# Kernel optimization log

Hardware: AMD Instinct MI355X
Metric: run time of the kernel (lower is better)

## Reference

```python
import jax, jax.numpy as jnp
import numpy as np

N = 100000       # n_entities + n_users
E = 1000000      # edges
D = 64           # entity_dim (phase/mod half-width)
R = 40           # n_relations
PI = 3.1415926235897933
GAMMA = 12.0
EMB_RANGE = (GAMMA + 2.0) / D   # (gamma + epsilon) / entity_dim
DIMS = [128, 64, 32, 16]        # conv_dim_list = [2*D] + [64,32,16]


def setup_inputs() -> dict:
    key = jax.random.key(0)
    ks = jax.random.split(key, 20)
    inp = {}
    inp["entity_embed"] = jax.random.uniform(ks[0], (N, 2 * D), minval=-EMB_RANGE, maxval=EMB_RANGE, dtype=jnp.float32)
    inp["rel_embed"] = jax.random.uniform(ks[1], (R, 3 * D), minval=-EMB_RANGE, maxval=EMB_RANGE, dtype=jnp.float32)
    inp["phase_w"] = jnp.array([[0.5 * EMB_RANGE]], dtype=jnp.float32)
    inp["mod_w"] = jnp.array([[1.0]], dtype=jnp.float32)
    names = [("W1_0", "b1_0", "W2_0", "b2_0"), ("W1_1", "b1_1", "W2_1", "b2_1"), ("W1_2", "b1_2", "W1_2b", "b2_2")]
    for i, (w1n, b1n, w2n, b2n) in enumerate(names):
        din, dout = DIMS[i], DIMS[i + 1]
        s = 1.0 / np.sqrt(din)
        inp[w1n] = jax.random.uniform(ks[2 + 4 * i], (dout, din), minval=-s, maxval=s, dtype=jnp.float32)
        inp[b1n] = jax.random.uniform(ks[3 + 4 * i], (dout,), minval=-s, maxval=s, dtype=jnp.float32)
        inp[w2n] = jax.random.uniform(ks[4 + 4 * i], (dout, din), minval=-s, maxval=s, dtype=jnp.float32)
        inp[b2n] = jax.random.uniform(ks[5 + 4 * i], (dout,), minval=-s, maxval=s, dtype=jnp.float32)
    inp["src"] = jax.random.randint(ks[14], (E,), 0, N, dtype=jnp.int32)
    inp["dst"] = jax.random.randint(ks[15], (E,), 0, N, dtype=jnp.int32)
    inp["etype"] = jax.random.randint(ks[16], (E,), 0, R, dtype=jnp.int32)
    return inp


def _edge_att(entity_embed, rel_embed, phase_w, mod_w, src, dst, etype):
    # HAKE att_score: h = dst node, t = src node (per original code)
    h = entity_embed[dst]            # [E, 2D]
    t = entity_embed[src]            # [E, 2D]
    r = rel_embed[etype]             # [E, 3D]
    scale = EMB_RANGE / PI
    ph, mh = h[:, :D], h[:, D:]
    pr, mr, br = r[:, :D], r[:, D:2 * D], r[:, 2 * D:]
    pt, mt = t[:, :D], t[:, D:]
    mr = jnp.abs(mr)
    br = jnp.minimum(br, 1.0)
    br = jnp.where(br < -mr, -mr, br)  # conditional write bias_relation[indicator] = -mod_relation
    mod_score = jnp.linalg.norm(mh * (mr + br) - mt * (1.0 - br), axis=1) * mod_w[0, 0]
    phase = (ph + pr - pt) / scale
    phase_score = jnp.sum(jnp.abs(jnp.sin(phase / 2.0)), axis=1) * phase_w[0, 0]
    att = phase_score + mod_score    # [E]
    # edge softmax over incoming edges of each dst node
    amax = jax.ops.segment_max(att, dst, num_segments=N)
    ex = jnp.exp(att - amax[dst])
    den = jax.ops.segment_sum(ex, dst, num_segments=N)
    return ex / den[dst]


def reference(entity_embed, rel_embed, phase_w, mod_w,
              W1_0, b1_0, W2_0, b2_0,
              W1_1, b1_1, W2_1, b2_1,
              W1_2, b1_2, W1_2b, b2_2,
              src, dst, etype):
    att = _edge_att(entity_embed, rel_embed, phase_w, mod_w, src, dst, etype)

    def layer(node, W1, b1, W2, b2):
        # u_mul_e('node','att','side') + sum('side','N_h')
        msg = node[src] * att[:, None]                    # [E, din]
        Nh = jax.ops.segment_sum(msg, dst, num_segments=N)
        # bi-interaction aggregator
        o = jax.nn.leaky_relu((node + Nh) @ W1.T + b1) + jax.nn.leaky_relu((node * Nh) @ W2.T + b2)
        nrm = jnp.linalg.norm(o, axis=1, keepdims=True)
        return o, o / jnp.maximum(nrm, 1e-12)             # (ego_embed, F.normalize)

    ego = entity_embed
    outs = [ego]
    for (W1, b1, W2, b2) in [(W1_0, b1_0, W2_0, b2_0), (W1_1, b1_1, W2_1, b2_1), (W1_2, b1_2, W1_2b, b2_2)]:
        ego, normed = layer(ego, W1, b1, W2, b2)
        outs.append(normed)
    return jnp.concatenate(outs, axis=1)                   # [N, 128+64+32+16]
```

## Files before the change

kernel.cpp:

```cpp
#include <hip/hip_runtime.h>
#include <math.h>


__global__ void hist_kernel(const int* __restrict__ dst, int* __restrict__ cnt,
                            int nedges) {
    int e = blockIdx.x * blockDim.x + threadIdx.x;
    if (e < nedges) atomicAdd(&cnt[dst[e]], 1);
}

__global__ __launch_bounds__(1024) void scan_block_kernel(
    const int* __restrict__ cnt, int* __restrict__ rowptr,
    int* __restrict__ bsum, int n) {
    __shared__ int swv[16];
    int tid = threadIdx.x, lane = tid & 63, wid = tid >> 6;
    int i = blockIdx.x * 1024 + tid;
    int v = (i < n) ? cnt[i] : 0;
    #pragma unroll
    for (int off = 1; off < 64; off <<= 1) {
        int t = __shfl_up(v, off, 64);
        if (lane >= off) v += t;
    }
    if (lane == 63) swv[wid] = v;
    __syncthreads();
    if (wid == 0) {
        int s = (lane < 16) ? swv[lane] : 0;
        #pragma unroll
        for (int off = 1; off < 16; off <<= 1) {
            int t = __shfl_up(s, off, 64);
            if (lane >= off) s += t;
        }
        if (lane < 16) swv[lane] = s;
    }
    __syncthreads();
    int offv = wid ? swv[wid - 1] : 0;
    if (i < n) rowptr[i + 1] = v + offv;
    if (tid == 1023) bsum[blockIdx.x] = v + offv;
}

__global__ __launch_bounds__(64) void scan_tops_kernel(
    const int* __restrict__ bsum, int* __restrict__ boff, int nb) {
    int l = threadIdx.x;
    int a = (2 * l < nb) ? bsum[2 * l] : 0;
    int b = (2 * l + 1 < nb) ? bsum[2 * l + 1] : 0;
    int s = a + b;
    #pragma unroll
    for (int off = 1; off < 64; off <<= 1) {
        int t = __shfl_up(s, off, 64);
        if (l >= off) s += t;
    }
    int excl = s - (a + b);
    if (2 * l < nb) boff[2 * l] = excl;
    if (2 * l + 1 < nb) boff[2 * l + 1] = excl + a;
}

__global__ __launch_bounds__(1024) void scan_add_kernel(
    int* __restrict__ rowptr, const int* __restrict__ boff, int n) {
    int i = blockIdx.x * 1024 + threadIdx.x;
    if (i < n) rowptr[i + 1] += boff[blockIdx.x];
    if (i == 0) rowptr[0] = 0;
}

__global__ void fill_kernel(const int* __restrict__ src, const int* __restrict__ dst,
                            const int* __restrict__ etype,
                            const int* __restrict__ rowptr, int* __restrict__ cursor,
                            int* __restrict__ se_s, int nedges) {
    int e = blockIdx.x * blockDim.x + threadIdx.x;
    if (e >= nedges) return;
    int d = dst[e];
    int slot = rowptr[d] + atomicAdd(&cursor[d], 1);
    se_s[slot] = src[e] | (etype[e] << 17);
}

__global__ __launch_bounds__(512) void att_gather_kernel(
    const float* __restrict__ embed, const float* __restrict__ rel,
    const float* __restrict__ pw, const float* __restrict__ mw,
    const int* __restrict__ se_s, const int* __restrict__ rowptr,
    float* __restrict__ att_s, float* __restrict__ ai,
    float* __restrict__ Nh, int nnodes, int nrel)
{
    __shared__ float sRel[40 * 196];
    int tid = threadIdx.x;

    for (int idx = tid; idx < nrel * 64; idx += 512) {
        int r = idx >> 6, d = idx & 63;
        float pr = rel[r * 192 + d];
        float mr = fabsf(rel[r * 192 + 64 + d]);
        float br = rel[r * 192 + 128 + d];
        br = fminf(br, 1.0f);
        br = fmaxf(br, -mr);
        sRel[r * 196 + d]       = mr + br;
        sRel[r * 196 + 64 + d]  = 1.0f - br;
        sRel[r * 196 + 128 + d] = pr;
    }
    __syncthreads();

    const float K = (float)(0.5 * 3.1415926235897933 / 0.21875);
    float mwv = mw[0], pwv = pw[0];

    int wave = tid >> 6, lane = tid & 63;
    int g = lane >> 4;
    int q = lane & 15;

    for (int v = blockIdx.x * 8 + wave; v < nnodes; v += gridDim.x * 8) {
        int beg = rowptr[v];
        int deg = rowptr[v + 1] - beg;

        const float* hrow = embed + (size_t)v * 128;
        float4 hp = *(const float4*)(hrow + 4 * q);
        float4 hm = *(const float4*)(hrow + 64 + 4 * q);

        float den = 0.0f;
        float4 accp = make_float4(0.f, 0.f, 0.f, 0.f);
        float4 accm = make_float4(0.f, 0.f, 0.f, 0.f);

        for (int kb = 0; kb < deg; kb += 64) {
            int kchunk = min(64, deg - kb);
            int sev = (lane < kchunk) ? se_s[beg + kb + lane] : 0;

            bool valid0 = g < kchunk;
            int se0 = __shfl(sev, valid0 ? g : 0, 64);
            int r0 = se0 >> 17;
            const float* trow0 = embed + (size_t)(se0 & 0x1FFFF) * 128;
            float4 tp0 = *(const float4*)(trow0 + 4 * q);
            float4 tm0 = *(const float4*)(trow0 + 64 + 4 * q);

            for (int k0 = 0; k0 < kchunk; k0 += 4) {
                float4 tp1 = tp0, tm1 = tm0;
                int r1 = r0;
                bool valid1 = false;
                if (k0 + 4 < kchunk) {
                    int kn = k0 + 4 + g;
                    valid1 = kn < kchunk;
                    int se1 = __shfl(sev, valid1 ? kn : 0, 64);
                    r1 = se1 >> 17;
                    const float* trow1 = embed + (size_t)(se1 & 0x1FFFF) * 128;
                    tp1 = *(const float4*)(trow1 + 4 * q);
                    tm1 = *(const float4*)(trow1 + 64 + 4 * q);
                }

                const float* rrow = sRel + r0 * 196;
                float4 A4 = *(const float4*)(rrow + 4 * q);
                float4 B4 = *(const float4*)(rrow + 64 + 4 * q);
                float4 P4 = *(const float4*)(rrow + 128 + 4 * q);

                float pp;
                pp  = fabsf(__sinf((hp.x + P4.x - tp0.x) * K));
                pp += fabsf(__sinf((hp.y + P4.y - tp0.y) * K));
                pp += fabsf(__sinf((hp.z + P4.z - tp0.z) * K));
                pp += fabsf(__sinf((hp.w + P4.w - tp0.w) * K));

                float d0 = hm.x * A4.x - tm0.x * B4.x;
                float d1 = hm.y * A4.y - tm0.y * B4.y;
                float d2 = hm.z * A4.z - tm0.z * B4.z;
                float d3 = hm.w * A4.w - tm0.w * B4.w;
                float qq = (d0 * d0 + d1 * d1) + (d2 * d2 + d3 * d3);

                #pragma unroll
                for (int off = 1; off < 16; off <<= 1) {
                    pp += __shfl_xor(pp, off, 64);
                    qq += __shfl_xor(qq, off, 64);
                }
                float s = sqrtf(qq) * mwv + pp * pwv;
                float w = valid0 ? __expf(s) : 0.0f;
                den += w;
                accp.x = fmaf(w, tp0.x, accp.x); accp.y = fmaf(w, tp0.y, accp.y);
                accp.z = fmaf(w, tp0.z, accp.z); accp.w = fmaf(w, tp0.w, accp.w);
                accm.x = fmaf(w, tm0.x, accm.x); accm.y = fmaf(w, tm0.y, accm.y);
                accm.z = fmaf(w, tm0.z, accm.z); accm.w = fmaf(w, tm0.w, accm.w);
                if (valid0 && q == 0) att_s[beg + kb + k0 + g] = w;

                tp0 = tp1; tm0 = tm1; r0 = r1; valid0 = valid1;
            }
        }

        #pragma unroll
        for (int off = 16; off < 64; off <<= 1) {
            accp.x += __shfl_xor(accp.x, off, 64);
            accp.y += __shfl_xor(accp.y, off, 64);
            accp.z += __shfl_xor(accp.z, off, 64);
            accp.w += __shfl_xor(accp.w, off, 64);
            accm.x += __shfl_xor(accm.x, off, 64);
            accm.y += __shfl_xor(accm.y, off, 64);
            accm.z += __shfl_xor(accm.z, off, 64);
            accm.w += __shfl_xor(accm.w, off, 64);
            den += __shfl_xor(den, off, 64);
        }
        float invd = (deg > 0) ? 1.0f / den : 0.0f;
        if (g == 0) {
            float* pn = Nh + (size_t)v * 128;
            *(float4*)(pn + 4 * q) = make_float4(accp.x * invd, accp.y * invd,
                                                 accp.z * invd, accp.w * invd);
            *(float4*)(pn + 64 + 4 * q) = make_float4(accm.x * invd, accm.y * invd,
                                                      accm.z * invd, accm.w * invd);
            if (q == 0) ai[v] = invd;
        }
    }
}

template<int DIN>
__global__ __launch_bounds__(256) void gather_kernel(
    const float* __restrict__ node, int nstride, const float* __restrict__ nrm,
    const float* __restrict__ att_s, const int* __restrict__ se_s,
    const int* __restrict__ rowptr, const float* __restrict__ ai,
    float* __restrict__ Nh, int nnodes)
{
    constexpr int LPE = DIN / 4;
    constexpr int EP  = 64 / LPE;
    constexpr int U   = 4;
    int v = blockIdx.x * 4 + (threadIdx.x >> 6);
    if (v >= nnodes) return;
    int lane = threadIdx.x & 63;
    int sub = lane / LPE;
    int c = lane % LPE;
    int beg = rowptr[v];
    int deg = rowptr[v + 1] - beg;

    float4 acc = make_float4(0.f, 0.f, 0.f, 0.f);
    for (int kb = 0; kb < deg; kb += 64) {
        int kc = kb + lane;
        bool inr = kc < deg;
        int sv = inr ? (se_s[beg + kc] & 0x1FFFF) : 0;
        float av = inr ? att_s[beg + kc] * nrm[sv] : 0.0f;
        int kmax = min(64, deg - kb);
        for (int k0 = 0; k0 < kmax; k0 += U * EP) {
            float a[U];
            const float4* p[U];
            #pragma unroll
            for (int u = 0; u < U; ++u) {
                int kk = k0 + u * EP + sub;
                bool val = kk < kmax;
                int kidx = val ? kk : 0;
                int ssrc = __shfl(sv, kidx, 64);
                float aa = __shfl(av, kidx, 64);
                a[u] = val ? aa : 0.0f;
                p[u] = (const float4*)(node + (size_t)ssrc * nstride + 4 * c);
            }
            float4 rv[U];
            #pragma unroll
            for (int u = 0; u < U; ++u) rv[u] = *p[u];
            #pragma unroll
            for (int u = 0; u < U; ++u) {
                acc.x += a[u] * rv[u].x;
                acc.y += a[u] * rv[u].y;
                acc.z += a[u] * rv[u].z;
                acc.w += a[u] * rv[u].w;
            }
        }
    }
    #pragma unroll
    for (int off = LPE; off < 64; off <<= 1) {
        acc.x += __shfl_xor(acc.x, off, 64);
        acc.y += __shfl_xor(acc.y, off, 64);
        acc.z += __shfl_xor(acc.z, off, 64);
        acc.w += __shfl_xor(acc.w, off, 64);
    }
    if (sub == 0) {
        float aiv = ai[v];
        float4 o = make_float4(acc.x * aiv, acc.y * aiv,
                               acc.z * aiv, acc.w * aiv);
        *(float4*)(Nh + (size_t)v * DIN + 4 * c) = o;
    }
}

template<int DIN, int DOUT, bool NRM, bool EGO>
__global__ __launch_bounds__(512) void gemm_kernel(
    const float* __restrict__ node, int nstride, const float* __restrict__ nrm_in,
    const float* __restrict__ Nh,
    const float* __restrict__ W1, const float* __restrict__ b1,
    const float* __restrict__ W2, const float* __restrict__ b2,
    float* __restrict__ out, int out_col, float* __restrict__ nrm_out, int nnodes)
{
    constexpr int IH  = (DIN < 64) ? DIN : 64;
    constexpr int NHV = DIN / IH;
    constexpr int XS  = IH + 1;
    constexpr int CPR = IH / 8;
    constexpr int DH  = DOUT / 8;
    __shared__ float sx1[64 * XS], sx2[64 * XS];
    __shared__ float sred[8][64];

    int tid = threadIdx.x;
    int tile0 = blockIdx.x * 64;
    int lane = tid & 63;
    int jh = __builtin_amdgcn_readfirstlane(tid >> 6);
    int j0 = jh * DH;
    int v = tile0 + lane;
    bool act = v < nnodes;

    float acc1[DH], acc2[DH];
    #pragma unroll
    for (int j = 0; j < DH; ++j) { acc1[j] = 0.f; acc2[j] = 0.f; }

    const float* px1 = sx1 + lane * XS;
    const float* px2 = sx2 + lane * XS;

    #pragma unroll
    for (int h = 0; h < NHV; ++h) {
        const int i0 = h * IH;
        if (h) __syncthreads();

        for (int idx = tid; idx < 64 * CPR; idx += 512) {
            int row = idx / CPR, c = idx % CPR;
            int vv = tile0 + row;
            float4 n0 = make_float4(0.f, 0.f, 0.f, 0.f), n1 = n0;
            float4 h0 = n0, h1 = n0;
            if (vv < nnodes) {
                const float* pn = node + (size_t)vv * nstride + i0 + 8 * c;
                const float* ph = Nh + (size_t)vv * DIN + i0 + 8 * c;
                n0 = *(const float4*)pn;
                n1 = *(const float4*)(pn + 4);
                h0 = *(const float4*)ph;
                h1 = *(const float4*)(ph + 4);
                if (EGO) {
                    float* po = out + (size_t)vv * 240 + i0 + 8 * c;
                    *(float4*)po = n0;
                    *(float4*)(po + 4) = n1;
                }
                if (NRM) {
                    float rn = nrm_in[vv];
                    n0.x *= rn; n0.y *= rn; n0.z *= rn; n0.w *= rn;
                    n1.x *= rn; n1.y *= rn; n1.z *= rn; n1.w *= rn;
                }
            }
            float* p1 = sx1 + row * XS + 8 * c;
            float* p2 = sx2 + row * XS + 8 * c;
            p1[0] = n0.x + h0.x; p1[1] = n0.y + h0.y;
            p1[2] = n0.z + h0.z; p1[3] = n0.w + h0.w;
            p1[4] = n1.x + h1.x; p1[5] = n1.y + h1.y;
            p1[6] = n1.z + h1.z; p1[7] = n1.w + h1.w;
            p2[0] = n0.x * h0.x; p2[1] = n0.y * h0.y;
            p2[2] = n0.z * h0.z; p2[3] = n0.w * h0.w;
            p2[4] = n1.x * h1.x; p2[5] = n1.y * h1.y;
            p2[6] = n1.z * h1.z; p2[7] = n1.w * h1.w;
        }
        __syncthreads();

        #pragma unroll 1
        for (int ic = 0; ic < IH; ic += 8) {
            float x1c[8], x2c[8];
            #pragma unroll
            for (int t = 0; t < 8; ++t) {
                x1c[t] = px1[ic + t];
                x2c[t] = px2[ic + t];
            }
            #pragma unroll
            for (int j = 0; j < DH; ++j) {
                const float* w1 = W1 + (size_t)(j0 + j) * DIN + i0 + ic;
                const float* w2 = W2 + (size_t)(j0 + j) * DIN + i0 + ic;
                #pragma unroll
                for (int t = 0; t < 8; ++t) {
                    acc1[j] = fmaf(x1c[t], w1[t], acc1[j]);
                    acc2[j] = fmaf(x2c[t], w2[t], acc2[j]);
                }
            }
        }
    }

    float o[DH];
    float ss = 0.0f;
    #pragma unroll
    for (int j = 0; j < DH; ++j) {
        float a1 = acc1[j] + b1[j0 + j];
        a1 = a1 >= 0.0f ? a1 : 0.01f * a1;
        float a2 = acc2[j] + b2[j0 + j];
        a2 = a2 >= 0.0f ? a2 : 0.01f * a2;
        o[j] = a1 + a2;
        ss += o[j] * o[j];
    }
    sred[jh][lane] = ss;
    __syncthreads();
    float tot = 0.0f;
    #pragma unroll
    for (int q = 0; q < 8; ++q) tot += sred[q][lane];
    float nv2 = fmaxf(sqrtf(tot), 1e-12f);
    float inv = 1.0f / nv2;
    if (act) {
        float* po = out + (size_t)v * 240 + out_col + j0;
        if (DH >= 4) {
            #pragma unroll
            for (int j = 0; j < DH; j += 4) {
                float4 st = make_float4(o[j] * inv, o[j + 1] * inv,
                                        o[j + 2] * inv, o[j + 3] * inv);
                *(float4*)(po + j) = st;
            }
        } else {
            #pragma unroll
            for (int j = 0; j < DH; ++j) po[j] = o[j] * inv;
        }
        if (nrm_out && jh == 0) nrm_out[v] = nv2;
    }
}

extern "C" void kernel_launch(void* const* d_in, const int* in_sizes, int n_in,
                              void* d_out, int out_size, void* d_ws, size_t ws_size,
                              hipStream_t stream) {
    const float* embed = (const float*)d_in[0];
    const float* rel   = (const float*)d_in[1];
    const float* pw    = (const float*)d_in[2];
    const float* mw    = (const float*)d_in[3];
    const float* W1_0  = (const float*)d_in[4];
    const float* b1_0  = (const float*)d_in[5];
    const float* W2_0  = (const float*)d_in[6];
    const float* b2_0  = (const float*)d_in[7];
    const float* W1_1  = (const float*)d_in[8];
    const float* b1_1  = (const float*)d_in[9];
    const float* W2_1  = (const float*)d_in[10];
    const float* b2_1  = (const float*)d_in[11];
    const float* W1_2  = (const float*)d_in[12];
    const float* b1_2  = (const float*)d_in[13];
    const float* W1_2b = (const float*)d_in[14];
    const float* b2_2  = (const float*)d_in[15];
    const int* src   = (const int*)d_in[16];
    const int* dst   = (const int*)d_in[17];
    const int* etype = (const int*)d_in[18];
    float* out = (float*)d_out;

    const int n = in_sizes[0] / 128;
    const int e = in_sizes[16];
    const int r = in_sizes[1] / 192;

    char* ws = (char*)d_ws;
    float* att_s  = (float*)ws;
    int*   se_s   = (int*)(att_s + e);
    float* Nh     = (float*)(se_s + e);
    int*   rowptr = (int*)(Nh + (size_t)n * 128);
    int*   cnt    = rowptr + n + 1;
    int*   cursor = cnt + n;
    int*   bsum   = cursor + n;
    int*   boff   = bsum + 128;
    float* nrm1   = (float*)(boff + 128);
    float* nrm2   = nrm1 + n;
    float* ai     = nrm2 + n;

    const int NB = (n + 1023) / 1024;

    hipMemsetAsync(cnt, 0, (size_t)(2 * n) * 4, stream);
    hist_kernel<<<(e + 255) / 256, 256, 0, stream>>>(dst, cnt, e);
    scan_block_kernel<<<NB, 1024, 0, stream>>>(cnt, rowptr, bsum, n);
    scan_tops_kernel<<<1, 64, 0, stream>>>(bsum, boff, NB);
    scan_add_kernel<<<NB, 1024, 0, stream>>>(rowptr, boff, n);
    fill_kernel<<<(e + 255) / 256, 256, 0, stream>>>(src, dst, etype, rowptr,
                                                     cursor, se_s, e);

    int gblocks = (n + 3) / 4;
    int tiles = (n + 63) / 64;

    att_gather_kernel<<<1024, 512, 0, stream>>>(
        embed, rel, pw, mw, se_s, rowptr, att_s, ai, Nh, n, r);

    gemm_kernel<128, 64, false, true><<<tiles, 512, 0, stream>>>(
        embed, 128, nullptr, Nh, W1_0, b1_0, W2_0, b2_0, out, 128, nrm1, n);
    gather_kernel<64><<<gblocks, 256, 0, stream>>>(
        out + 128, 240, nrm1, att_s, se_s, rowptr, ai, Nh, n);
    gemm_kernel<64, 32, true, false><<<tiles, 512, 0, stream>>>(
        out + 128, 240, nrm1, Nh, W1_1, b1_1, W2_1, b2_1, out, 192, nrm2, n);
    gather_kernel<32><<<gblocks, 256, 0, stream>>>(
        out + 192, 240, nrm2, att_s, se_s, rowptr, ai, Nh, n);
    gemm_kernel<32, 16, true, false><<<tiles, 512, 0, stream>>>(
        out + 192, 240, nrm2, Nh, W1_2, b1_2, W1_2b, b2_2, out, 224, nullptr, n);
}
```

Measured before the change: 440.3 us.

## Fuse neighbor gather with bi-interaction GEMM for layers 1 and 2

Replaces the separate gather and GEMM kernels for the second and third layers with one fused kernel. Each block gathers the weighted neighbor sums for its 64-node tile straight into shared memory, forms the sum and product inputs, then runs the dense transform, leaky-relu and normalization. This removes the Nh round trip through global memory and two kernel launches. In exchange, each wave gathers 8 rows one after another and the GEMM phase waits on a block barrier. The node index is also made wave-uniform with readfirstlane so its loads can go through the scalar path.

```diff
diff --git a/kernel.cpp b/kernel.cpp
--- a/kernel.cpp
+++ b/kernel.cpp
@@ -102,10 +102,11 @@
     int q = lane & 15;
 
     for (int v = blockIdx.x * 8 + wave; v < nnodes; v += gridDim.x * 8) {
-        int beg = rowptr[v];
-        int deg = rowptr[v + 1] - beg;
-
-        const float* hrow = embed + (size_t)v * 128;
+        int vu = __builtin_amdgcn_readfirstlane(v);
+        int beg = rowptr[vu];
+        int deg = rowptr[vu + 1] - beg;
+
+        const float* hrow = embed + (size_t)vu * 128;
         float4 hp = *(const float4*)(hrow + 4 * q);
         float4 hm = *(const float4*)(hrow + 64 + 4 * q);
 
@@ -187,78 +188,163 @@
         }
         float invd = (deg > 0) ? 1.0f / den : 0.0f;
         if (g == 0) {
-            float* pn = Nh + (size_t)v * 128;
+            float* pn = Nh + (size_t)vu * 128;
             *(float4*)(pn + 4 * q) = make_float4(accp.x * invd, accp.y * invd,
                                                  accp.z * invd, accp.w * invd);
             *(float4*)(pn + 64 + 4 * q) = make_float4(accm.x * invd, accm.y * invd,
                                                       accm.z * invd, accm.w * invd);
-            if (q == 0) ai[v] = invd;
-        }
-    }
-}
-
-template<int DIN>
-__global__ __launch_bounds__(256) void gather_kernel(
-    const float* __restrict__ node, int nstride, const float* __restrict__ nrm,
+            if (q == 0) ai[vu] = invd;
+        }
+    }
+}
+
+template<int DIN, int DOUT>
+__global__ __launch_bounds__(512) void fused_layer_kernel(
+    const float* __restrict__ node, int nstride, const float* __restrict__ nrm_in,
     const float* __restrict__ att_s, const int* __restrict__ se_s,
     const int* __restrict__ rowptr, const float* __restrict__ ai,
-    float* __restrict__ Nh, int nnodes)
+    const float* __restrict__ W1, const float* __restrict__ b1,
+    const float* __restrict__ W2, const float* __restrict__ b2,
+    float* __restrict__ out, int out_col, float* __restrict__ nrm_out, int nnodes)
 {
+    constexpr int XS  = DIN + 1;
     constexpr int LPE = DIN / 4;
     constexpr int EP  = 64 / LPE;
     constexpr int U   = 4;
-    int v = blockIdx.x * 4 + (threadIdx.x >> 6);
-    if (v >= nnodes) return;
-    int lane = threadIdx.x & 63;
-    int sub = lane / LPE;
-    int c = lane % LPE;
-    int beg = rowptr[v];
-    int deg = rowptr[v + 1] - beg;
-
-    float4 acc = make_float4(0.f, 0.f, 0.f, 0.f);
-    for (int kb = 0; kb < deg; kb += 64) {
-        int kc = kb + lane;
-        bool inr = kc < deg;
-        int sv = inr ? (se_s[beg + kc] & 0x1FFFF) : 0;
-        float av = inr ? att_s[beg + kc] * nrm[sv] : 0.0f;
-        int kmax = min(64, deg - kb);
-        for (int k0 = 0; k0 < kmax; k0 += U * EP) {
-            float a[U];
-            const float4* p[U];
-            #pragma unroll
-            for (int u = 0; u < U; ++u) {
-                int kk = k0 + u * EP + sub;
-                bool val = kk < kmax;
-                int kidx = val ? kk : 0;
-                int ssrc = __shfl(sv, kidx, 64);
-                float aa = __shfl(av, kidx, 64);
-                a[u] = val ? aa : 0.0f;
-                p[u] = (const float4*)(node + (size_t)ssrc * nstride + 4 * c);
-            }
-            float4 rv[U];
-            #pragma unroll
-            for (int u = 0; u < U; ++u) rv[u] = *p[u];
-            #pragma unroll
-            for (int u = 0; u < U; ++u) {
-                acc.x += a[u] * rv[u].x;
-                acc.y += a[u] * rv[u].y;
-                acc.z += a[u] * rv[u].z;
-                acc.w += a[u] * rv[u].w;
-            }
-        }
-    }
-    #pragma unroll
-    for (int off = LPE; off < 64; off <<= 1) {
-        acc.x += __shfl_xor(acc.x, off, 64);
-        acc.y += __shfl_xor(acc.y, off, 64);
-        acc.z += __shfl_xor(acc.z, off, 64);
-        acc.w += __shfl_xor(acc.w, off, 64);
-    }
-    if (sub == 0) {
-        float aiv = ai[v];
-        float4 o = make_float4(acc.x * aiv, acc.y * aiv,
-                               acc.z * aiv, acc.w * aiv);
-        *(float4*)(Nh + (size_t)v * DIN + 4 * c) = o;
+    constexpr int DH  = DOUT / 8;
+    __shared__ float sx1[64 * XS], sx2[64 * XS];
+    __shared__ float sred[8][64];
+
+    int tid = threadIdx.x, lane = tid & 63, wave = tid >> 6;
+    int tile0 = blockIdx.x * 64;
+    int sub = lane / LPE, c = lane % LPE;
+
+    for (int rr = 0; rr < 8; ++rr) {
+        int row = wave * 8 + rr;
+        int v = tile0 + row;
+        if (v >= nnodes) break;
+        int vu = __builtin_amdgcn_readfirstlane(v);
+        int beg = rowptr[vu];
+        int deg = rowptr[vu + 1] - beg;
+
+        float4 acc = make_float4(0.f, 0.f, 0.f, 0.f);
+        for (int kb = 0; kb < deg; kb += 64) {
+            int kc = kb + lane;
+            bool inr = kc < deg;
+            int sv = inr ? (se_s[beg + kc] & 0x1FFFF) : 0;
+            float av = inr ? att_s[beg + kc] * nrm_in[sv] : 0.0f;
+            int kmax = min(64, deg - kb);
+            for (int k0 = 0; k0 < kmax; k0 += U * EP) {
+                float a[U];
+                const float4* p[U];
+                #pragma unroll
+                for (int u = 0; u < U; ++u) {
+                    int kk = k0 + u * EP + sub;
+                    bool val = kk < kmax;
+                    int kidx = val ? kk : 0;
+                    int ssrc = __shfl(sv, kidx, 64);
+                    float aa = __shfl(av, kidx, 64);
+                    a[u] = val ? aa : 0.0f;
+                    p[u] = (const float4*)(node + (size_t)ssrc * nstride + 4 * c);
+                }
+                float4 rv[U];
+                #pragma unroll
+                for (int u = 0; u < U; ++u) rv[u] = *p[u];
+                #pragma unroll
+                for (int u = 0; u < U; ++u) {
+                    acc.x += a[u] * rv[u].x;
+                    acc.y += a[u] * rv[u].y;
+                    acc.z += a[u] * rv[u].z;
+                    acc.w += a[u] * rv[u].w;
+                }
+            }
+        }
+        #pragma unroll
+        for (int off = LPE; off < 64; off <<= 1) {
+            acc.x += __shfl_xor(acc.x, off, 64);
+            acc.y += __shfl_xor(acc.y, off, 64);
+            acc.z += __shfl_xor(acc.z, off, 64);
+            acc.w += __shfl_xor(acc.w, off, 64);
+        }
+        if (sub == 0) {
+            float aiv = ai[vu];
+            float rn = nrm_in[vu];
+            float4 nv4 = *(const float4*)(node + (size_t)vu * nstride + 4 * c);
+            nv4.x *= rn; nv4.y *= rn; nv4.z *= rn; nv4.w *= rn;
+            acc.x *= aiv; acc.y *= aiv; acc.z *= aiv; acc.w *= aiv;
+            float* p1 = sx1 + row * XS + 4 * c;
+            float* p2 = sx2 + row * XS + 4 * c;
+            p1[0] = nv4.x + acc.x; p1[1] = nv4.y + acc.y;
+            p1[2] = nv4.z + acc.z; p1[3] = nv4.w + acc.w;
+            p2[0] = nv4.x * acc.x; p2[1] = nv4.y * acc.y;
+            p2[2] = nv4.z * acc.z; p2[3] = nv4.w * acc.w;
+        }
+    }
+    __syncthreads();
+
+    int jh = __builtin_amdgcn_readfirstlane(wave);
+    int j0 = jh * DH;
+    int v = tile0 + lane;
+    bool act = v < nnodes;
+
+    float acc1[DH], acc2[DH];
+    #pragma unroll
+    for (int j = 0; j < DH; ++j) { acc1[j] = 0.f; acc2[j] = 0.f; }
+
+    const float* px1 = sx1 + lane * XS;
+    const float* px2 = sx2 + lane * XS;
+    #pragma unroll 1
+    for (int ic = 0; ic < DIN; ic += 8) {
+        float x1c[8], x2c[8];
+        #pragma unroll
+        for (int t = 0; t < 8; ++t) {
+            x1c[t] = px1[ic + t];
+            x2c[t] = px2[ic + t];
+        }
+        #pragma unroll
+        for (int j = 0; j < DH; ++j) {
+            const float* w1 = W1 + (size_t)(j0 + j) * DIN + ic;
+            const float* w2 = W2 + (size_t)(j0 + j) * DIN + ic;
+            #pragma unroll
+            for (int t = 0; t < 8; ++t) {
+                acc1[j] = fmaf(x1c[t], w1[t], acc1[j]);
+                acc2[j] = fmaf(x2c[t], w2[t], acc2[j]);
+            }
+        }
+    }
+
+    float o[DH];
+    float ss = 0.0f;
+    #pragma unroll
+    for (int j = 0; j < DH; ++j) {
+        float a1 = acc1[j] + b1[j0 + j];
+        a1 = a1 >= 0.0f ? a1 : 0.01f * a1;
+        float a2 = acc2[j] + b2[j0 + j];
+        a2 = a2 >= 0.0f ? a2 : 0.01f * a2;
+        o[j] = a1 + a2;
+        ss += o[j] * o[j];
+    }
+    sred[jh][lane] = ss;
+    __syncthreads();
+    float tot = 0.0f;
+    #pragma unroll
+    for (int qq = 0; qq < 8; ++qq) tot += sred[qq][lane];
+    float nv2 = fmaxf(sqrtf(tot), 1e-12f);
+    float inv = 1.0f / nv2;
+    if (act) {
+        float* po = out + (size_t)v * 240 + out_col + j0;
+        if (DH >= 4) {
+            #pragma unroll
+            for (int j = 0; j < DH; j += 4) {
+                float4 st = make_float4(o[j] * inv, o[j + 1] * inv,
+                                        o[j + 2] * inv, o[j + 3] * inv);
+                *(float4*)(po + j) = st;
+            }
+        } else {
+            #pragma unroll
+            for (int j = 0; j < DH; ++j) po[j] = o[j] * inv;
+        }
+        if (nrm_out && jh == 0) nrm_out[v] = nv2;
     }
 }
 
@@ -441,7 +527,6 @@
     fill_kernel<<<(e + 255) / 256, 256, 0, stream>>>(src, dst, etype, rowptr,
                                                      cursor, se_s, e);
 
-    int gblocks = (n + 3) / 4;
     int tiles = (n + 63) / 64;
 
     att_gather_kernel<<<1024, 512, 0, stream>>>(
@@ -449,12 +534,10 @@
 
     gemm_kernel<128, 64, false, true><<<tiles, 512, 0, stream>>>(
         embed, 128, nullptr, Nh, W1_0, b1_0, W2_0, b2_0, out, 128, nrm1, n);
-    gather_kernel<64><<<gblocks, 256, 0, stream>>>(
-        out + 128, 240, nrm1, att_s, se_s, rowptr, ai, Nh, n);
-    gemm_kernel<64, 32, true, false><<<tiles, 512, 0, stream>>>(
-        out + 128, 240, nrm1, Nh, W1_1, b1_1, W2_1, b2_1, out, 192, nrm2, n);
-    gather_kernel<32><<<gblocks, 256, 0, stream>>>(
-        out + 192, 240, nrm2, att_s, se_s, rowptr, ai, Nh, n);
-    gemm_kernel<32, 16, true, false><<<tiles, 512, 0, stream>>>(
-        out + 192, 240, nrm2, Nh, W1_2, b1_2, W1_2b, b2_2, out, 224, nullptr, n);
-}
+    fused_layer_kernel<64, 32><<<tiles, 512, 0, stream>>>(
+        out + 128, 240, nrm1, att_s, se_s, rowptr, ai,
+        W1_1, b1_1, W2_1, b2_1, out, 192, nrm2, n);
+    fused_layer_kernel<32, 16><<<tiles, 512, 0, stream>>>(
+        out + 192, 240, nrm2, att_s, se_s, rowptr, ai,
+        W1_2, b1_2, W1_2b, b2_2, out, 224, nullptr, n);
+}
```

New measurement: 437.4 us. No clear change (-0.7%).
